# Kernel optimization log

Measured on AMD Instinct MI355X. Metric: run time of the kernel, lower is better.

## Reference

```python
import jax, jax.numpy as jnp
import numpy as np

N_NODES = 100000
BN_EPS = 1e-5


def _linear_params(key, fan_in, fan_out):
    k1, k2 = jax.random.split(key)
    lim = 1.0 / np.sqrt(fan_in)
    W = jax.random.uniform(k1, (fan_in, fan_out), jnp.float32, -lim, lim)
    b = jax.random.uniform(k2, (fan_out,), jnp.float32, -lim, lim)
    return W, b


def setup_inputs() -> dict:
    key = jax.random.key(0)
    ks = jax.random.split(key, 24)
    in_ch, hid, tdim, L = 17, 64, 32, 2
    E = 1600000
    inp = {}
    inp["x"] = jax.random.normal(ks[0], (N_NODES, in_ch), jnp.float32)
    inp["edge_index"] = jax.random.randint(ks[1], (2, E), 0, N_NODES, jnp.int64)
    inp["edge_dts"] = jax.random.uniform(ks[2], (E,), jnp.float32) * 100.0
    inp["batch_size"] = 10000
    # TimeEncode params (learned, TGAT init)
    inp["basis_freq"] = jnp.asarray(1.0 / 10 ** np.linspace(0, 9, tdim), jnp.float32)
    inp["phase"] = jnp.zeros((tdim,), jnp.float32)
    # TMP edge MLP: in = 2*in_ch + tdim
    mi = 2 * in_ch + tdim
    inp["tmp_W1"], inp["tmp_b1"] = _linear_params(ks[3], mi, mi // 2)
    inp["tmp_W2"], inp["tmp_b2"] = _linear_params(ks[4], mi // 2, in_ch)
    inp["proj_W"], inp["proj_b"] = _linear_params(ks[5], in_ch, hid)
    # SMP layers (stacked over L)
    si = 2 * hid
    W1s, b1s, W2s, b2s = [], [], [], []
    for l in range(L):
        W1, b1 = _linear_params(ks[6 + 2 * l], si, si // 2)
        W2, b2 = _linear_params(ks[7 + 2 * l], si // 2, hid)
        W1s.append(W1); b1s.append(b1); W2s.append(W2); b2s.append(b2)
    inp["smp_W1"] = jnp.stack(W1s); inp["smp_b1"] = jnp.stack(b1s)
    inp["smp_W2"] = jnp.stack(W2s); inp["smp_b2"] = jnp.stack(b2s)
    inp["bn_gamma"] = jnp.ones((L, hid), jnp.float32)
    inp["bn_beta"] = jnp.zeros((L, hid), jnp.float32)
    # classifier head
    inp["clf_W1"], inp["clf_b1"] = _linear_params(ks[12], hid, hid)
    inp["clf_g1"] = jnp.ones((hid,), jnp.float32); inp["clf_bb1"] = jnp.zeros((hid,), jnp.float32)
    inp["clf_W2"], inp["clf_b2"] = _linear_params(ks[13], hid, hid // 2)
    inp["clf_g2"] = jnp.ones((hid // 2,), jnp.float32); inp["clf_bb2"] = jnp.zeros((hid // 2,), jnp.float32)
    inp["clf_W3"], inp["clf_b3"] = _linear_params(ks[14], hid // 2, 1)
    return inp


def _segment_mean(vals, idx, n):
    s = jax.ops.segment_sum(vals, idx, num_segments=n)
    c = jax.ops.segment_sum(jnp.ones((idx.shape[0], 1), vals.dtype), idx, num_segments=n)
    return s / jnp.maximum(c, 1.0)


def _bn(x, g, b):
    m = x.mean(0)
    v = x.var(0)
    return (x - m) * jax.lax.rsqrt(v + BN_EPS) * g + b


def reference(x, edge_index, edge_dts, batch_size, basis_freq, phase,
              tmp_W1, tmp_b1, tmp_W2, tmp_b2, proj_W, proj_b,
              smp_W1, smp_b1, smp_W2, smp_b2, bn_gamma, bn_beta,
              clf_W1, clf_b1, clf_g1, clf_bb1,
              clf_W2, clf_b2, clf_g2, clf_bb2, clf_W3, clf_b3):
    src, dst = edge_index[0], edge_index[1]  # x_j = x[src], x_i = x[dst]
    n = x.shape[0]
    # TimeEncode: cos(t * freq + phase)  -> [E, time_dim]
    rel = jnp.cos(edge_dts[:, None] * basis_freq + phase)
    # --- TMP conv (applied once) ---
    x_i = x[dst]
    m_in = jnp.concatenate([x_i, x[src], rel], axis=-1)
    p = jnp.tanh(jax.nn.relu(m_in @ tmp_W1 + tmp_b1) @ tmp_W2 + tmp_b2)
    msg = (2.0 * p - 1.0) * x_i  # (p - q) * x_i with q = 1 - p
    h = x + _segment_mean(msg, dst, n)
    # --- project to hidden ---
    h = h @ proj_W + proj_b
    # --- L SMP layers with BatchNorm + ReLU (dropout = eval/identity) ---
    L = smp_W1.shape[0]
    for l in range(L):
        h_i = h[dst]
        m_in = jnp.concatenate([h_i, h[src]], axis=-1)
        p = jnp.tanh(jax.nn.relu(m_in @ smp_W1[l] + smp_b1[l]) @ smp_W2[l] + smp_b2[l])
        h = h + _segment_mean((2.0 * p - 1.0) * h_i, dst, n)
        h = jax.nn.relu(_bn(h, bn_gamma[l], bn_beta[l]))
    # --- classifier on seed nodes ---
    z = h[:batch_size]
    z = jax.nn.relu(_bn(z @ clf_W1 + clf_b1, clf_g1, clf_bb1))
    z = jax.nn.relu(_bn(z @ clf_W2 + clf_b2, clf_g2, clf_bb2))
    return z @ clf_W3 + clf_b3  # [batch_size, 1] logits
```

## Files before the change

kernel.cpp:

```cpp
#include <hip/hip_runtime.h>
#include <hip/hip_bf16.h>


typedef float  f32x4 __attribute__((ext_vector_type(4)));
typedef short  s16x8 __attribute__((ext_vector_type(8)));

__device__ __forceinline__ float tanh_factor(float u) {
  float e = __expf(2.0f * u);
  return fmaf(-4.0f, __builtin_amdgcn_rcpf(e + 1.0f), 1.0f);
}

__device__ __forceinline__ void atomic_add_f32(float* p, float v) {
  unsafeAtomicAdd(p, v);
}

__device__ __forceinline__ unsigned short f2bf(float f) {
  __hip_bfloat16 b = __float2bfloat16(f);
  return *(unsigned short*)&b;
}
__device__ __forceinline__ float bf2f(unsigned short u) {
  unsigned int v = ((unsigned int)u) << 16;
  return *(float*)&v;
}

__global__ __launch_bounds__(256) void k_hist(
    const int* __restrict__ ei, int* __restrict__ cntI, int E)
{
  int e = blockIdx.x * 256 + threadIdx.x;
  if (e < E) atomicAdd(&cntI[__builtin_nontemporal_load(ei + E + e)], 1);
}

__global__ __launch_bounds__(256) void k_scan_block(
    const int* __restrict__ cntI, int* __restrict__ cursor,
    int* __restrict__ bsum, int N)
{
  __shared__ int s[256];
  const int t = threadIdx.x;
  int i = blockIdx.x * 256 + t;
  int v = (i < N) ? cntI[i] : 0;
  s[t] = v;
  for (int off = 1; off < 256; off <<= 1) {
    __syncthreads();
    int x = (t >= off) ? s[t - off] : 0;
    __syncthreads();
    s[t] += x;
  }
  __syncthreads();
  if (i < N) cursor[i] = s[t] - v;
  if (t == 255) bsum[blockIdx.x] = s[255];
}

__global__ __launch_bounds__(512) void k_scan_bsum(int* __restrict__ bsum, int nb)
{
  __shared__ int s[512];
  const int t = threadIdx.x;
  int v = (t < nb) ? bsum[t] : 0;
  s[t] = v;
  for (int off = 1; off < 512; off <<= 1) {
    __syncthreads();
    int x = (t >= off) ? s[t - off] : 0;
    __syncthreads();
    s[t] += x;
  }
  __syncthreads();
  if (t < nb) bsum[t] = s[t] - v;
}

__global__ __launch_bounds__(256) void k_expand_add(
    int* __restrict__ cursor, const int* __restrict__ bsum,
    const int* __restrict__ cntI, int* __restrict__ dstS, int N)
{
  int n = blockIdx.x * 256 + threadIdx.x;
  if (n >= N) return;
  int cur = cursor[n] + bsum[blockIdx.x];
  cursor[n] = cur;
  int c = cntI[n];
  for (int i = 0; i < c; i++) dstS[cur + i] = n;
}

__global__ __launch_bounds__(256) void k_scatter_x(
    const int* __restrict__ ei, const float* __restrict__ dts,
    int* __restrict__ cursor, int2* __restrict__ srcdtS, int E, int N)
{
  const int g  = blockIdx.x & 7;
  const int bi = blockIdx.x >> 3;
  const int nb = gridDim.x >> 3;
  const int lo = (int)(((long long)N * g) >> 3);
  const int hi = (int)(((long long)N * (g + 1)) >> 3);
  for (int e = bi * 256 + threadIdx.x; e < E; e += nb * 256) {
    int d = __builtin_nontemporal_load(ei + E + e);
    if (d >= lo && d < hi) {
      int s = __builtin_nontemporal_load(ei + e);
      float dt = __builtin_nontemporal_load(dts + e);
      int pos = atomicAdd(&cursor[d], 1);
      srcdtS[pos] = make_int2(s, __float_as_int(dt));
    }
  }
}

__global__ __launch_bounds__(256) void prep_all(
    const float* __restrict__ x, const float* __restrict__ tW1,
    const float* __restrict__ tW2, const float* __restrict__ sW1,
    const float* __restrict__ sW2, const float* __restrict__ cW1,
    const float* __restrict__ cW2, unsigned short* __restrict__ xb,
    unsigned short* __restrict__ W1t1, unsigned short* __restrict__ W2t1,
    unsigned short* __restrict__ W1t, unsigned short* __restrict__ W2t,
    unsigned short* __restrict__ cW1t, unsigned short* __restrict__ cW2t, int N)
{
  int i = blockIdx.x * 256 + threadIdx.x;
  int totalX = N * 24;
  for (int idx = i; idx < totalX; idx += gridDim.x * 256) {
    int n = idx / 24, c = idx - n * 24;
    xb[idx] = (c < 17) ? f2bf(x[n * 17 + c]) : (unsigned short)0;
  }
  if (i < 48 * 96) {
    int n = i / 96, k = i - n * 96;
    int src = (k < 17) ? k : (k >= 24 && k < 41) ? (k - 24 + 17)
            : (k >= 48 && k < 80) ? (k - 48 + 34) : -1;
    W1t1[i] = (n < 33 && src >= 0) ? f2bf(tW1[src * 33 + n]) : (unsigned short)0;
  }
  if (i < 32 * 64) {
    int n = i / 64, k = i - n * 64;
    W2t1[i] = (n < 17 && k < 33) ? f2bf(tW2[k * 17 + n]) : (unsigned short)0;
  }
  if (i < 2 * 64 * 128) {
    int l = i >> 13; int r = i & 8191; int n = r >> 7; int k = r & 127;
    W1t[i] = f2bf(sW1[((size_t)l * 128 + k) * 64 + n]);
  }
  if (i < 2 * 64 * 64) {
    int l = i >> 12; int r = i & 4095; int n = r >> 6; int k = r & 63;
    W2t[i] = f2bf(sW2[((size_t)l * 64 + k) * 64 + n]);
  }
  if (i < 64 * 64) {
    int c = i >> 6, k = i & 63;
    cW1t[i] = f2bf(cW1[k * 64 + c]);
  }
  if (i < 32 * 64) {
    int c = i >> 6, k = i & 63;
    cW2t[i] = f2bf(cW2[k * 32 + c]);
  }
}

__global__ __launch_bounds__(256, 3) void phase1_edge_mfma(
    const unsigned short* __restrict__ xb, const int* __restrict__ dstS,
    const int2* __restrict__ srcdtS, const float* __restrict__ freq,
    const float* __restrict__ phs,
    const unsigned short* __restrict__ W1t1, const float* __restrict__ b1,
    const unsigned short* __restrict__ W2t1, const float* __restrict__ b2,
    float* __restrict__ accum, int E, int nwt)
{
  __shared__ unsigned short sA[64][104];
  __shared__ unsigned short sHid[64][72];
  __shared__ float sRed[64][20];
  __shared__ int   sDst[64];

  const int t = threadIdx.x;
  const int wv = t >> 6, lane = t & 63, l16 = lane & 15, quad = lane >> 4;
  const int r0 = wv * 16;
  const int e_loc = lane >> 2, q = lane & 3;
  const int rr = r0 + e_loc;

  s16x8 w1f[3][3], w2f[2][2];
  float bias1[3], bias2[2];
#pragma unroll
  for (int cb = 0; cb < 3; cb++) {
    int n = cb * 16 + l16;
#pragma unroll
    for (int kb = 0; kb < 3; kb++)
      w1f[cb][kb] = *(const s16x8*)&W1t1[n * 96 + kb * 32 + quad * 8];
    bias1[cb] = (n < 33) ? b1[n] : 0.0f;
  }
#pragma unroll
  for (int cb = 0; cb < 2; cb++) {
    int n = cb * 16 + l16;
#pragma unroll
    for (int kb = 0; kb < 2; kb++)
      w2f[cb][kb] = *(const s16x8*)&W2t1[n * 64 + kb * 32 + quad * 8];
    bias2[cb] = (n < 17) ? b2[n] : 0.0f;
  }

  float frq[8], phv[8];
#pragma unroll
  for (int j = 0; j < 8; j++) {
    frq[j] = freq[q * 8 + j];
    phv[j] = phs[q * 8 + j];
  }

  for (int i = lane; i < 16 * 28; i += 64) {
    int rrz = r0 + i / 28, c = i % 28;
    int col = (c < 6) ? 18 + c : (c < 12) ? 42 + (c - 6) : 80 + (c - 12);
    sA[rrz][col] = 0;
  }
  for (int i = lane; i < 256; i += 64)
    sHid[r0 + (i >> 4)][48 + (i & 15)] = 0;

  const int g8   = blockIdx.x & 7;
  const int tLo  = (int)(((long long)nwt * g8) >> 3);
  const int tHi  = (int)(((long long)nwt * (g8 + 1)) >> 3);
  const int wLoc = (blockIdx.x >> 3) * 4 + wv;
  const int nwLoc = (gridDim.x >> 3) * 4;

  int ndP = 0; uint4 xa0, xa1; unsigned int xa2 = 0; float dtP = 0.0f;
  auto issue = [&](int tt) {
    int er = (tt << 4) + e_loc; if (er >= E) er = E - 1;
    if (q < 2) {
      ndP = q ? srcdtS[er].x : dstS[er];
      const unsigned short* src = &xb[(size_t)ndP * 24];
      xa0 = *(const uint4*)&src[0];
      xa1 = *(const uint4*)&src[8];
      xa2 = *(const unsigned int*)&src[16];
    }
    dtP = __int_as_float(srcdtS[er].y);
  };
  {
    int t0 = tLo + wLoc; if (t0 >= nwt) t0 = nwt - 1;
    issue(t0);
  }

  for (int tile = tLo + wLoc; tile < tHi; tile += nwLoc) {
    const int eb = tile << 4;

    if (q < 2) {
      if (!q) sDst[rr] = ndP;
      const int base = q ? 24 : 0;
      *(uint4*)&sA[rr][base]     = xa0;
      *(uint4*)&sA[rr][base + 8] = xa1;
      *(unsigned int*)&sA[rr][base + 16] = xa2;
    }
    {
      unsigned short tmp[8] __attribute__((aligned(16)));
#pragma unroll
      for (int j = 0; j < 8; j++)
        tmp[j] = f2bf(__cosf(fmaf(dtP, frq[j], phv[j])));
      *(uint4*)&sA[rr][48 + q * 8] = *(const uint4*)&tmp[0];
    }

    { int nt = tile + nwLoc; issue(nt < tHi ? nt : tile); }

    f32x4 a1[3];
#pragma unroll
    for (int cb = 0; cb < 3; cb++)
      a1[cb] = (f32x4){bias1[cb], bias1[cb], bias1[cb], bias1[cb]};
#pragma unroll
    for (int kb = 0; kb < 3; kb++) {
      s16x8 aF = *(const s16x8*)&sA[r0 + l16][kb * 32 + quad * 8];
#pragma unroll
      for (int cb = 0; cb < 3; cb++)
        a1[cb] = __builtin_amdgcn_mfma_f32_16x16x32_bf16(aF, w1f[cb][kb], a1[cb], 0, 0, 0);
    }
#pragma unroll
    for (int cb = 0; cb < 3; cb++)
#pragma unroll
      for (int reg = 0; reg < 4; reg++)
        sHid[r0 + quad * 4 + reg][cb * 16 + l16] = f2bf(fmaxf(a1[cb][reg], 0.0f));

    f32x4 a2[2];
#pragma unroll
    for (int cb = 0; cb < 2; cb++)
      a2[cb] = (f32x4){bias2[cb], bias2[cb], bias2[cb], bias2[cb]};
#pragma unroll
    for (int kb = 0; kb < 2; kb++) {
      s16x8 aF = *(const s16x8*)&sHid[r0 + l16][kb * 32 + quad * 8];
#pragma unroll
      for (int cb = 0; cb < 2; cb++)
        a2[cb] = __builtin_amdgcn_mfma_f32_16x16x32_bf16(aF, w2f[cb][kb], a2[cb], 0, 0, 0);
    }

#pragma unroll
    for (int reg = 0; reg < 4; reg++) {
      int row = r0 + quad * 4 + reg;
      bool ok = (eb + quad * 4 + reg < E);
      sRed[row][l16] = ok ? tanh_factor(a2[0][reg]) : 0.0f;
      if (l16 == 0) sRed[row][16] = ok ? tanh_factor(a2[1][reg]) : 0.0f;
    }

    if (lane < 17) {
      int col = lane;
      float run = 0.0f;
      int cur = __builtin_amdgcn_readfirstlane(sDst[r0]);
#pragma unroll
      for (int k = 0; k < 16; k++) {
        int d = __builtin_amdgcn_readfirstlane(sDst[r0 + k]);
        float v = sRed[r0 + k][col];
        if (d != cur) {
          atomic_add_f32(&accum[(size_t)cur * 17 + col], run);
          run = 0.0f; cur = d;
        }
        run += v;
      }
      atomic_add_f32(&accum[(size_t)cur * 17 + col], run);
    }
  }
}

__global__ __launch_bounds__(256) void phase1_node(
    const float* __restrict__ x, const float* __restrict__ acc1,
    const int* __restrict__ cntI, const float* __restrict__ Wp,
    const float* __restrict__ bp, float* __restrict__ h,
    float* __restrict__ acc2, int N)
{
  __shared__ float s0[4][20];
  const int t = threadIdx.x;
  const int nb = blockIdx.x << 2;
  if (t < 68) {
    int nl = t / 17, c = t % 17;
    int n = nb + nl;
    float v = 0.0f;
    if (n < N) {
      float cnt = fmaxf((float)cntI[n], 1.0f);
      v = x[n * 17 + c] * (1.0f + acc1[n * 17 + c] / cnt);
    }
    s0[nl][c] = v;
  }
  __syncthreads();
  int nl = t >> 6, j = t & 63;
  int n = nb + nl;
  if (n < N) {
    float acc = bp[j];
#pragma unroll
    for (int c = 0; c < 17; c++) acc = fmaf(s0[nl][c], Wp[c * 64 + j], acc);
    h[n * 64 + j] = acc;
    acc2[n * 64 + j] = 0.0f;
  }
}

template <bool DO_BN>
__global__ void prep_P(
    float* __restrict__ h, const unsigned short* __restrict__ W1t,
    const float* __restrict__ b1,
    const float* __restrict__ bns, const float* __restrict__ bnq,
    const float* __restrict__ gam, const float* __restrict__ bet, float invR,
    unsigned short* __restrict__ P1, unsigned short* __restrict__ P2, int N)
{
  __shared__ unsigned short sH[64][72];
  __shared__ float sM[64], sS[64], sB[64];
  const int t = threadIdx.x;
  const int wv = t >> 6, lane = t & 63, l16 = lane & 15, quad = lane >> 4;
  const int nb = blockIdx.x << 6;

  if (DO_BN) {
    if (t < 64) {
      float m = bns[t] * invR;
      float var = bnq[t] * invR - m * m;
      sM[t] = m;
      sS[t] = gam[t] * rsqrtf(var + 1e-5f);
      sB[t] = bet[t];
    }
    __syncthreads();
  }

#pragma unroll
  for (int i = 0; i < 4; i++) {
    int g = t + i * 256;
    int r = g >> 4, c4 = (g & 15) << 2;
    int n0 = nb + r;
    bool valid = (n0 < N);
    int n = valid ? n0 : N - 1;
    float4 v = *(const float4*)&h[(size_t)n * 64 + c4];
    if (DO_BN) {
      v.x = fmaxf(fmaf(v.x - sM[c4 + 0], sS[c4 + 0], sB[c4 + 0]), 0.0f);
      v.y = fmaxf(fmaf(v.y - sM[c4 + 1], sS[c4 + 1], sB[c4 + 1]), 0.0f);
      v.z = fmaxf(fmaf(v.z - sM[c4 + 2], sS[c4 + 2], sB[c4 + 2]), 0.0f);
      v.w = fmaxf(fmaf(v.w - sM[c4 + 3], sS[c4 + 3], sB[c4 + 3]), 0.0f);
      if (valid) *(float4*)&h[(size_t)n0 * 64 + c4] = v;
    }
    ushort4 o = { f2bf(v.x), f2bf(v.y), f2bf(v.z), f2bf(v.w) };
    *(ushort4*)&sH[r][c4] = o;
  }
  __syncthreads();

  const int n = nb + wv * 16 + l16;
#pragma unroll
  for (int half = 0; half < 2; half++) {
    f32x4 acc[4];
#pragma unroll
    for (int cb = 0; cb < 4; cb++) {
      if (half == 0) {
        float4 bv = *(const float4*)&b1[cb * 16 + quad * 4];
        acc[cb] = (f32x4){bv.x, bv.y, bv.z, bv.w};
      } else {
        acc[cb] = (f32x4){0.0f, 0.0f, 0.0f, 0.0f};
      }
    }
#pragma unroll
    for (int kb = 0; kb < 2; kb++) {
      s16x8 bF = *(const s16x8*)&sH[wv * 16 + l16][kb * 32 + quad * 8];
#pragma unroll
      for (int cb = 0; cb < 4; cb++) {
        s16x8 aF = *(const s16x8*)&W1t[(cb * 16 + l16) * 128 + half * 64 + kb * 32 + quad * 8];
        acc[cb] = __builtin_amdgcn_mfma_f32_16x16x32_bf16(aF, bF, acc[cb], 0, 0, 0);
      }
    }
    if (n < N) {
      unsigned short* P = half ? P2 : P1;
#pragma unroll
      for (int cb = 0; cb < 4; cb++) {
        ushort4 o = { f2bf(acc[cb][0]), f2bf(acc[cb][1]),
                      f2bf(acc[cb][2]), f2bf(acc[cb][3]) };
        *(ushort4*)&P[(size_t)n * 64 + cb * 16 + quad * 4] = o;
      }
    }
  }
}

__global__ __launch_bounds__(256, 4) void phase2_edge(
    const unsigned short* __restrict__ P1, const unsigned short* __restrict__ P2,
    const int* __restrict__ dstS, const int2* __restrict__ srcdtS,
    const unsigned short* __restrict__ W2t, const float* __restrict__ b2,
    float* __restrict__ accum, int E, int nwt)
{
  __shared__ unsigned short sA[64][136];
  __shared__ int sDst[64];
  float* sRedF = (float*)&sA[0][0];

  const int t = threadIdx.x;
  const int wv = t >> 6, lane = t & 63, l16 = lane & 15, quad = lane >> 4;
  const int r0 = wv * 16;

  s16x8 w2f[4][2];
  f32x4 bias2v[4];
#pragma unroll
  for (int cb = 0; cb < 4; cb++) {
#pragma unroll
    for (int kb = 0; kb < 2; kb++)
      w2f[cb][kb] = *(const s16x8*)&W2t[(cb * 16 + l16) * 64 + kb * 32 + quad * 8];
    float4 bv = *(const float4*)&b2[cb * 16 + quad * 4];
    bias2v[cb] = (f32x4){bv.x, bv.y, bv.z, bv.w};
  }

  const int eRow = r0 + l16;

  const int e_loc = lane >> 2, q = lane & 3;
  const int rr = r0 + e_loc;
  const unsigned short* const Pb = (q < 2) ? P1 : P2;
  const int cb0 = q * 32;
  const size_t sub = (size_t)((q & 1) * 32);

  const int g8   = blockIdx.x & 7;
  const int tLo  = (int)(((long long)nwt * g8) >> 3);
  const int tHi  = (int)(((long long)nwt * (g8 + 1)) >> 3);
  const int wLoc = (blockIdx.x >> 3) * 4 + wv;
  const int nwLoc = (gridDim.x >> 3) * 4;

  int ndP = 0; uint4 pA, pB, pC, pD;
  auto issue = [&](int tt) {
    int er = (tt << 4) + e_loc; if (er >= E) er = E - 1;
    ndP = (q < 2) ? dstS[er] : srcdtS[er].x;
    const unsigned short* src = Pb + (size_t)ndP * 64 + sub;
    pA = *(const uint4*)&src[0];
    pB = *(const uint4*)&src[8];
    pC = *(const uint4*)&src[16];
    pD = *(const uint4*)&src[24];
  };
  {
    int t0 = tLo + wLoc; if (t0 >= nwt) t0 = nwt - 1;
    issue(t0);
  }

  for (int tile = tLo + wLoc; tile < tHi; tile += nwLoc) {
    const int eb = tile << 4;

    if (q == 0) sDst[rr] = ndP;
    *(uint4*)&sA[rr][cb0]      = pA;
    *(uint4*)&sA[rr][cb0 + 8]  = pB;
    *(uint4*)&sA[rr][cb0 + 16] = pC;
    *(uint4*)&sA[rr][cb0 + 24] = pD;

    { int nt = tile + nwLoc; issue(nt < tHi ? nt : tile); }

    s16x8 hidf[2];
#pragma unroll
    for (int kb = 0; kb < 2; kb++) {
      s16x8 x1 = *(const s16x8*)&sA[eRow][kb * 32 + quad * 8];
      s16x8 x2 = *(const s16x8*)&sA[eRow][64 + kb * 32 + quad * 8];
      s16x8 hf;
#pragma unroll
      for (int j = 0; j < 8; j++) {
        float a = bf2f((unsigned short)x1[j]);
        float b = bf2f((unsigned short)x2[j]);
        hf[j] = (short)f2bf(fmaxf(a + b, 0.0f));
      }
      hidf[kb] = hf;
    }

    f32x4 acc[4];
#pragma unroll
    for (int cb = 0; cb < 4; cb++) acc[cb] = bias2v[cb];
#pragma unroll
    for (int kb = 0; kb < 2; kb++)
#pragma unroll
      for (int cb = 0; cb < 4; cb++)
        acc[cb] = __builtin_amdgcn_mfma_f32_16x16x32_bf16(w2f[cb][kb], hidf[kb], acc[cb], 0, 0, 0);

    bool ok = (eb + l16 < E);
#pragma unroll
    for (int cb = 0; cb < 4; cb++) {
      f32x4 f;
#pragma unroll
      for (int reg = 0; reg < 4; reg++)
        f[reg] = ok ? tanh_factor(acc[cb][reg]) : 0.0f;
      *(f32x4*)&sRedF[eRow * 68 + cb * 16 + quad * 4] = f;
    }

    {
      float run = 0.0f;
      int cur = __builtin_amdgcn_readfirstlane(sDst[r0]);
#pragma unroll
      for (int k = 0; k < 16; k++) {
        int d = __builtin_amdgcn_readfirstlane(sDst[r0 + k]);
        float v = sRedF[(r0 + k) * 68 + lane];
        if (d != cur) {
          atomic_add_f32(&accum[(size_t)cur * 64 + lane], run);
          run = 0.0f; cur = d;
        }
        run += v;
      }
      atomic_add_f32(&accum[(size_t)cur * 64 + lane], run);
    }
  }
}

__global__ __launch_bounds__(256) void node_update_bn(
    float* __restrict__ h, float* __restrict__ accum,
    const int* __restrict__ cntI, float* __restrict__ bns,
    float* __restrict__ bnq, int N)
{
  const int t = threadIdx.x;
  float ls = 0.0f, lq = 0.0f;
  int total = N * 64;
  for (int idx = blockIdx.x * 256 + t; idx < total; idx += gridDim.x * 256) {
    int n = idx >> 6;
    float cnt = fmaxf((float)cntI[n], 1.0f);
    float v = h[idx] * (1.0f + accum[idx] / cnt);
    accum[idx] = 0.0f;
    h[idx] = v;
    ls += v; lq += v * v;
  }
  __shared__ float ss[256], sq[256];
  ss[t] = ls; sq[t] = lq;
  __syncthreads();
  if (t < 64) {
    float s = ss[t] + ss[t + 64] + ss[t + 128] + ss[t + 192];
    float q = sq[t] + sq[t + 64] + sq[t + 128] + sq[t + 192];
    atomic_add_f32(&bns[t], s);
    atomic_add_f32(&bnq[t], q);
  }
}

template <int NCB>
__global__ __launch_bounds__(256) void clf_mfma(
    const float* __restrict__ in, const unsigned short* __restrict__ Wt,
    const float* __restrict__ bias, float* __restrict__ z,
    float* __restrict__ bns, float* __restrict__ bnq,
    const float* __restrict__ ibns, const float* __restrict__ ibnq,
    const float* __restrict__ igam, const float* __restrict__ ibet,
    float iinvR, int rows)
{
  __shared__ unsigned short sIn[64][72];
  __shared__ float sM[64], sS[64], sB[64];
  const int t = threadIdx.x;
  const int wv = t >> 6, lane = t & 63, l16 = lane & 15, quad = lane >> 4;
  const int nb = blockIdx.x << 6;

  if (t < 64) {
    float m = ibns[t] * iinvR;
    float var = ibnq[t] * iinvR - m * m;
    sM[t] = m;
    sS[t] = igam[t] * rsqrtf(var + 1e-5f);
    sB[t] = ibet[t];
  }

  s16x8 wf[NCB][2];
  f32x4 bv[NCB];
#pragma unroll
  for (int cb = 0; cb < NCB; cb++) {
#pragma unroll
    for (int kb = 0; kb < 2; kb++)
      wf[cb][kb] = *(const s16x8*)&Wt[(cb * 16 + l16) * 64 + kb * 32 + quad * 8];
    float4 b4 = *(const float4*)&bias[cb * 16 + quad * 4];
    bv[cb] = (f32x4){b4.x, b4.y, b4.z, b4.w};
  }
  __syncthreads();

#pragma unroll
  for (int i = 0; i < 4; i++) {
    int g = t + i * 256;
    int r = g >> 4, c4 = (g & 15) << 2;
    int n = nb + r; if (n >= rows) n = rows - 1;
    float4 v = *(const float4*)&in[(size_t)n * 64 + c4];
    v.x = fmaxf(fmaf(v.x - sM[c4 + 0], sS[c4 + 0], sB[c4 + 0]), 0.0f);
    v.y = fmaxf(fmaf(v.y - sM[c4 + 1], sS[c4 + 1], sB[c4 + 1]), 0.0f);
    v.z = fmaxf(fmaf(v.z - sM[c4 + 2], sS[c4 + 2], sB[c4 + 2]), 0.0f);
    v.w = fmaxf(fmaf(v.w - sM[c4 + 3], sS[c4 + 3], sB[c4 + 3]), 0.0f);
    ushort4 o = { f2bf(v.x), f2bf(v.y), f2bf(v.z), f2bf(v.w) };
    *(ushort4*)&sIn[r][c4] = o;
  }
  __syncthreads();

  const int n = nb + wv * 16 + l16;
  const bool ok = (n < rows);
  f32x4 acc[NCB];
#pragma unroll
  for (int cb = 0; cb < NCB; cb++) acc[cb] = bv[cb];
#pragma unroll
  for (int kb = 0; kb < 2; kb++) {
    s16x8 bF = *(const s16x8*)&sIn[wv * 16 + l16][kb * 32 + quad * 8];
#pragma unroll
    for (int cb = 0; cb < NCB; cb++)
      acc[cb] = __builtin_amdgcn_mfma_f32_16x16x32_bf16(wf[cb][kb], bF, acc[cb], 0, 0, 0);
  }

#pragma unroll
  for (int cb = 0; cb < NCB; cb++) {
    if (ok)
      *(float4*)&z[(size_t)n * (NCB * 16) + cb * 16 + quad * 4] =
          make_float4(acc[cb][0], acc[cb][1], acc[cb][2], acc[cb][3]);
    f32x4 s, q;
#pragma unroll
    for (int reg = 0; reg < 4; reg++) {
      float v = ok ? acc[cb][reg] : 0.0f;
      s[reg] = v; q[reg] = v * v;
    }
#pragma unroll
    for (int m = 1; m < 16; m <<= 1) {
#pragma unroll
      for (int reg = 0; reg < 4; reg++) {
        s[reg] += __shfl_xor(s[reg], m);
        q[reg] += __shfl_xor(q[reg], m);
      }
    }
    if (l16 == 0) {
#pragma unroll
      for (int reg = 0; reg < 4; reg++) {
        int col = cb * 16 + quad * 4 + reg;
        atomic_add_f32(&bns[col], s[reg]);
        atomic_add_f32(&bnq[col], q[reg]);
      }
    }
  }
}

__global__ __launch_bounds__(256) void clf_final(
    const float* __restrict__ z2, const float* __restrict__ W3,
    const float* __restrict__ b3,
    const float* __restrict__ ibns, const float* __restrict__ ibnq,
    const float* __restrict__ igam, const float* __restrict__ ibet,
    float iinvR, float* __restrict__ out, int rows)
{
  __shared__ float sM[32], sS[32], sB[32];
  const int t = threadIdx.x;
  if (t < 32) {
    float m = ibns[t] * iinvR;
    float var = ibnq[t] * iinvR - m * m;
    sM[t] = m;
    sS[t] = igam[t] * rsqrtf(var + 1e-5f);
    sB[t] = ibet[t];
  }
  __syncthreads();
  int n = blockIdx.x * 256 + t;
  if (n >= rows) return;
  float acc = b3[0];
#pragma unroll
  for (int k = 0; k < 32; k++) {
    float v = fmaxf(fmaf(z2[n * 32 + k] - sM[k], sS[k], sB[k]), 0.0f);
    acc = fmaf(v, W3[k], acc);
  }
  out[n] = acc;
}

extern "C" void kernel_launch(void* const* d_in, const int* in_sizes, int n_in,
                              void* d_out, int out_size, void* d_ws, size_t ws_size,
                              hipStream_t stream)
{
  const float* x    = (const float*)d_in[0];
  const int*   ei   = (const int*)  d_in[1];
  const float* dts  = (const float*)d_in[2];
  const float* freq = (const float*)d_in[4];
  const float* phs  = (const float*)d_in[5];
  const float* tW1  = (const float*)d_in[6];
  const float* tb1  = (const float*)d_in[7];
  const float* tW2  = (const float*)d_in[8];
  const float* tb2  = (const float*)d_in[9];
  const float* pW   = (const float*)d_in[10];
  const float* pb   = (const float*)d_in[11];
  const float* sW1  = (const float*)d_in[12];
  const float* sb1  = (const float*)d_in[13];
  const float* sW2  = (const float*)d_in[14];
  const float* sb2  = (const float*)d_in[15];
  const float* bng  = (const float*)d_in[16];
  const float* bnb  = (const float*)d_in[17];
  const float* cW1  = (const float*)d_in[18];
  const float* cb1  = (const float*)d_in[19];
  const float* cg1  = (const float*)d_in[20];
  const float* cbb1 = (const float*)d_in[21];
  const float* cW2  = (const float*)d_in[22];
  const float* cb2  = (const float*)d_in[23];
  const float* cg2  = (const float*)d_in[24];
  const float* cbb2 = (const float*)d_in[25];
  const float* cW3  = (const float*)d_in[26];
  const float* cb3  = (const float*)d_in[27];
  float* out = (float*)d_out;

  const int N = in_sizes[0] / 17;
  const int E = in_sizes[1] / 2;
  const int B = out_size;

  char* base = (char*)d_ws;
  size_t off = 0;
  float* h    = (float*)(base + off); off += (size_t)N * 64 * 4;
  float* acc2 = (float*)(base + off); off += (size_t)N * 64 * 4;
  char*  uni  = base + off;           off += (size_t)N * 64 * 4;
  float* bnsAll = (float*)(base + off); off += 8 * 64 * 4;
  unsigned short* W1t = (unsigned short*)(base + off); off += 2 * 64 * 128 * 2;
  unsigned short* W2t = (unsigned short*)(base + off); off += 2 * 64 * 64 * 2;
  unsigned short* cW1t = (unsigned short*)(base + off); off += 64 * 64 * 2;
  unsigned short* cW2t = (unsigned short*)(base + off); off += 32 * 64 * 2;
  int* cntI   = (int*)(base + off); off += (size_t)N * 4;
  int* cursor = (int*)(base + off); off += (size_t)N * 4;
  int* bsum   = (int*)(base + off); off += 512 * 4;
  int* dstS   = (int*)(base + off); off += (size_t)E * 4;
  off = (off + 15) & ~(size_t)15;
  int2* srcdtS = (int2*)(base + off); off += (size_t)E * 8;
  size_t needed = off;
  if (ws_size < needed) return;

  float* acc1 = (float*)uni;
  unsigned short* xb   = (unsigned short*)(uni + (size_t)N * 17 * 4);
  unsigned short* W1t1 = xb + (size_t)N * 24;
  unsigned short* W2t1 = W1t1 + 48 * 96;
  unsigned short* P1 = (unsigned short*)uni;
  unsigned short* P2 = P1 + (size_t)N * 64;
  float* z1 = (float*)uni;
  float* z2 = z1 + (size_t)B * 64;

  const int nwt = (E + 15) / 16;
  const int NB = (N + 255) / 256;
  if (NB > 512) return;

  hipMemsetAsync(cntI, 0, (size_t)N * 4, stream);
  hipMemsetAsync(acc1, 0, (size_t)N * 17 * 4, stream);
  hipMemsetAsync(bnsAll, 0, 8 * 64 * 4, stream);

  k_hist<<<(E + 255) / 256, 256, 0, stream>>>(ei, cntI, E);
  k_scan_block<<<NB, 256, 0, stream>>>(cntI, cursor, bsum, N);
  k_scan_bsum<<<1, 512, 0, stream>>>(bsum, NB);
  k_expand_add<<<NB, 256, 0, stream>>>(cursor, bsum, cntI, dstS, N);
  k_scatter_x<<<1024, 256, 0, stream>>>(ei, dts, cursor, srcdtS, E, N);
  prep_all<<<(N * 24 + 255) / 256, 256, 0, stream>>>(
      x, tW1, tW2, sW1, sW2, cW1, cW2, xb, W1t1, W2t1, W1t, W2t, cW1t, cW2t, N);

  phase1_edge_mfma<<<768, 256, 0, stream>>>(
      xb, dstS, srcdtS, freq, phs, W1t1, tb1, W2t1, tb2, acc1, E, nwt);
  phase1_node<<<(N + 3) / 4, 256, 0, stream>>>(x, acc1, cntI, pW, pb, h, acc2, N);

  const int PB = (N + 63) / 64;
  prep_P<false><<<PB, 256, 0, stream>>>(
      h, W1t, sb1, nullptr, nullptr, nullptr, nullptr, 0.0f, P1, P2, N);
  phase2_edge<<<1024, 256, 0, stream>>>(
      P1, P2, dstS, srcdtS, W2t, sb2, acc2, E, nwt);
  node_update_bn<<<1024, 256, 0, stream>>>(h, acc2, cntI,
                                           bnsAll + 0, bnsAll + 64, N);
  prep_P<true><<<PB, 256, 0, stream>>>(
      h, W1t + (size_t)64 * 128, sb1 + 64, bnsAll + 0, bnsAll + 64,
      bng, bnb, 1.0f / (float)N, P1, P2, N);
  phase2_edge<<<1024, 256, 0, stream>>>(
      P1, P2, dstS, srcdtS, W2t + (size_t)64 * 64, sb2 + 64, acc2, E, nwt);
  node_update_bn<<<1024, 256, 0, stream>>>(h, acc2, cntI,
                                           bnsAll + 128, bnsAll + 192, N);

  const int CB = (B + 63) / 64;
  clf_mfma<4><<<CB, 256, 0, stream>>>(
      h, cW1t, cb1, z1, bnsAll + 256, bnsAll + 320,
      bnsAll + 128, bnsAll + 192, bng + 64, bnb + 64, 1.0f / (float)N, B);
  clf_mfma<2><<<CB, 256, 0, stream>>>(
      z1, cW2t, cb2, z2, bnsAll + 384, bnsAll + 448,
      bnsAll + 256, bnsAll + 320, cg1, cbb1, 1.0f / (float)B, B);
  clf_final<<<(B + 255) / 256, 256, 0, stream>>>(
      z2, cW3, cb3, bnsAll + 384, bnsAll + 448, cg2, cbb2,
      1.0f / (float)B, out, B);
}
```

Baseline: 814.1 us.

## Deepen edge-kernel prefetch to two stages and raise occupancy and grid size

Both edge kernels now fetch indices two tiles ahead and the gathered node payload one tile ahead. The index load is no longer serialized with the dependent gather in the same prefetch step. Launch bounds go up (phase1 3→4, phase2 4→5 blocks per CU), and the grids grow to match. This is meant to hide the latency of the dependent index→gather chain. The extra live registers under a tighter register cap could cause spills.

Result: no change. 800.1 us (-1.7%).

```diff
diff --git a/kernel.cpp b/kernel.cpp
--- a/kernel.cpp
+++ b/kernel.cpp
@@ -141,7 +141,7 @@
   }
 }
 
-__global__ __launch_bounds__(256, 3) void phase1_edge_mfma(
+__global__ __launch_bounds__(256, 4) void phase1_edge_mfma(
     const unsigned short* __restrict__ xb, const int* __restrict__ dstS,
     const int2* __restrict__ srcdtS, const float* __restrict__ freq,
     const float* __restrict__ phs,
@@ -200,21 +200,29 @@
   const int wLoc = (blockIdx.x >> 3) * 4 + wv;
   const int nwLoc = (gridDim.x >> 3) * 4;
 
+  int idxN = 0; float dtN = 0.0f;
   int ndP = 0; uint4 xa0, xa1; unsigned int xa2 = 0; float dtP = 0.0f;
-  auto issue = [&](int tt) {
+  auto issue_idx = [&](int tt) {
     int er = (tt << 4) + e_loc; if (er >= E) er = E - 1;
+    int2 sd = srcdtS[er];
+    idxN = q ? sd.x : dstS[er];
+    dtN  = __int_as_float(sd.y);
+  };
+  auto issue_payload = [&]() {
+    ndP = idxN; dtP = dtN;
     if (q < 2) {
-      ndP = q ? srcdtS[er].x : dstS[er];
       const unsigned short* src = &xb[(size_t)ndP * 24];
       xa0 = *(const uint4*)&src[0];
       xa1 = *(const uint4*)&src[8];
       xa2 = *(const unsigned int*)&src[16];
     }
-    dtP = __int_as_float(srcdtS[er].y);
   };
   {
     int t0 = tLo + wLoc; if (t0 >= nwt) t0 = nwt - 1;
-    issue(t0);
+    issue_idx(t0);
+    issue_payload();
+    int t1 = t0 + nwLoc; if (t1 >= tHi) t1 = t0;
+    issue_idx(t1);
   }
 
   for (int tile = tLo + wLoc; tile < tHi; tile += nwLoc) {
@@ -235,7 +243,8 @@
       *(uint4*)&sA[rr][48 + q * 8] = *(const uint4*)&tmp[0];
     }
 
-    { int nt = tile + nwLoc; issue(nt < tHi ? nt : tile); }
+    issue_payload();
+    { int nt = tile + 2 * nwLoc; issue_idx(nt < tHi ? nt : tile); }
 
     f32x4 a1[3];
 #pragma unroll
@@ -403,7 +412,7 @@
   }
 }
 
-__global__ __launch_bounds__(256, 4) void phase2_edge(
+__global__ __launch_bounds__(256, 5) void phase2_edge(
     const unsigned short* __restrict__ P1, const unsigned short* __restrict__ P2,
     const int* __restrict__ dstS, const int2* __restrict__ srcdtS,
     const unsigned short* __restrict__ W2t, const float* __restrict__ b2,
@@ -442,10 +451,14 @@
   const int wLoc = (blockIdx.x >> 3) * 4 + wv;
   const int nwLoc = (gridDim.x >> 3) * 4;
 
+  int idxN = 0;
   int ndP = 0; uint4 pA, pB, pC, pD;
-  auto issue = [&](int tt) {
+  auto issue_idx = [&](int tt) {
     int er = (tt << 4) + e_loc; if (er >= E) er = E - 1;
-    ndP = (q < 2) ? dstS[er] : srcdtS[er].x;
+    idxN = (q < 2) ? dstS[er] : srcdtS[er].x;
+  };
+  auto issue_payload = [&]() {
+    ndP = idxN;
     const unsigned short* src = Pb + (size_t)ndP * 64 + sub;
     pA = *(const uint4*)&src[0];
     pB = *(const uint4*)&src[8];
@@ -454,7 +467,10 @@
   };
   {
     int t0 = tLo + wLoc; if (t0 >= nwt) t0 = nwt - 1;
-    issue(t0);
+    issue_idx(t0);
+    issue_payload();
+    int t1 = t0 + nwLoc; if (t1 >= tHi) t1 = t0;
+    issue_idx(t1);
   }
 
   for (int tile = tLo + wLoc; tile < tHi; tile += nwLoc) {
@@ -466,7 +482,8 @@
     *(uint4*)&sA[rr][cb0 + 16] = pC;
     *(uint4*)&sA[rr][cb0 + 24] = pD;
 
-    { int nt = tile + nwLoc; issue(nt < tHi ? nt : tile); }
+    issue_payload();
+    { int nt = tile + 2 * nwLoc; issue_idx(nt < tHi ? nt : tile); }
 
     s16x8 hidf[2];
 #pragma unroll
@@ -749,21 +766,21 @@
   prep_all<<<(N * 24 + 255) / 256, 256, 0, stream>>>(
       x, tW1, tW2, sW1, sW2, cW1, cW2, xb, W1t1, W2t1, W1t, W2t, cW1t, cW2t, N);
 
-  phase1_edge_mfma<<<768, 256, 0, stream>>>(
+  phase1_edge_mfma<<<1024, 256, 0, stream>>>(
       xb, dstS, srcdtS, freq, phs, W1t1, tb1, W2t1, tb2, acc1, E, nwt);
   phase1_node<<<(N + 3) / 4, 256, 0, stream>>>(x, acc1, cntI, pW, pb, h, acc2, N);
 
   const int PB = (N + 63) / 64;
   prep_P<false><<<PB, 256, 0, stream>>>(
       h, W1t, sb1, nullptr, nullptr, nullptr, nullptr, 0.0f, P1, P2, N);
-  phase2_edge<<<1024, 256, 0, stream>>>(
+  phase2_edge<<<1280, 256, 0, stream>>>(
       P1, P2, dstS, srcdtS, W2t, sb2, acc2, E, nwt);
   node_update_bn<<<1024, 256, 0, stream>>>(h, acc2, cntI,
                                            bnsAll + 0, bnsAll + 64, N);
   prep_P<true><<<PB, 256, 0, stream>>>(
       h, W1t + (size_t)64 * 128, sb1 + 64, bnsAll + 0, bnsAll + 64,
       bng, bnb, 1.0f / (float)N, P1, P2, N);
-  phase2_edge<<<1024, 256, 0, stream>>>(
+  phase2_edge<<<1280, 256, 0, stream>>>(
       P1, P2, dstS, srcdtS, W2t + (size_t)64 * 64, sb2 + 64, acc2, E, nwt);
   node_update_bn<<<1024, 256, 0, stream>>>(h, acc2, cntI,
                                            bnsAll + 128, bnsAll + 192, N);
```

## Deepen gather prefetch pipeline in edge kernels with two tiles in flight

Applied to the files above, without the earlier changes.

Both edge kernels now process tile pairs per iteration. They keep two payload gathers in flight and prefetch the index loads two steps ahead, so the dependent index-then-payload gather latency is hidden better. phase2_edge also raises its occupancy hint to 5 blocks per SM and launches 1280 blocks instead of 1024. The deeper pipeline costs more registers, and that could hurt occupancy or cause spills. The work split changes too, with each wave starting at tLo+2*wLoc and striding by 2*S.

Result: slower. 982.1 us (+20.6%).

```diff
diff --git a/kernel.cpp b/kernel.cpp
--- a/kernel.cpp
+++ b/kernel.cpp
@@ -198,97 +198,184 @@
   const int tLo  = (int)(((long long)nwt * g8) >> 3);
   const int tHi  = (int)(((long long)nwt * (g8 + 1)) >> 3);
   const int wLoc = (blockIdx.x >> 3) * 4 + wv;
-  const int nwLoc = (gridDim.x >> 3) * 4;
-
-  int ndP = 0; uint4 xa0, xa1; unsigned int xa2 = 0; float dtP = 0.0f;
-  auto issue = [&](int tt) {
+  const int S    = (gridDim.x >> 3) * 4;
+  const int tp0  = tLo + 2 * wLoc;
+
+  int iA = 0, iB = 0, jA = 0, jB = 0;
+  float dA = 0.0f, dB = 0.0f, eA = 0.0f, eB = 0.0f;
+  uint4 a0 = {0,0,0,0}, a1 = {0,0,0,0}, b0 = {0,0,0,0}, b1v = {0,0,0,0};
+  unsigned int a2v = 0, b2v = 0;
+
+  auto clampT = [&](int tt) { return tt < tHi ? tt : tHi - 1; };
+  auto ld_idx = [&](int tt, int& ix, float& dt) {
     int er = (tt << 4) + e_loc; if (er >= E) er = E - 1;
+    int2 sd = srcdtS[er];
+    ix = q ? sd.x : dstS[er];
+    dt = __int_as_float(sd.y);
+  };
+  auto ld_pay = [&](int ix, uint4& x0, uint4& x1, unsigned int& x2) {
     if (q < 2) {
-      ndP = q ? srcdtS[er].x : dstS[er];
-      const unsigned short* src = &xb[(size_t)ndP * 24];
-      xa0 = *(const uint4*)&src[0];
-      xa1 = *(const uint4*)&src[8];
-      xa2 = *(const unsigned int*)&src[16];
-    }
-    dtP = __int_as_float(srcdtS[er].y);
+      const unsigned short* src = &xb[(size_t)ix * 24];
+      x0 = *(const uint4*)&src[0];
+      x1 = *(const uint4*)&src[8];
+      x2 = *(const unsigned int*)&src[16];
+    }
   };
-  {
-    int t0 = tLo + wLoc; if (t0 >= nwt) t0 = nwt - 1;
-    issue(t0);
-  }
-
-  for (int tile = tLo + wLoc; tile < tHi; tile += nwLoc) {
-    const int eb = tile << 4;
-
-    if (q < 2) {
-      if (!q) sDst[rr] = ndP;
-      const int base = q ? 24 : 0;
-      *(uint4*)&sA[rr][base]     = xa0;
-      *(uint4*)&sA[rr][base + 8] = xa1;
-      *(unsigned int*)&sA[rr][base + 16] = xa2;
-    }
+
+  if (tp0 < tHi) {
+    ld_idx(tp0, iA, dA);
+    ld_idx(clampT(tp0 + 1), iB, dB);
+    ld_pay(iA, a0, a1, a2v);
+    ld_pay(iB, b0, b1v, b2v);
+    ld_idx(clampT(tp0 + 2 * S), jA, eA);
+    ld_idx(clampT(tp0 + 2 * S + 1), jB, eB);
+  }
+
+  for (int tp = tp0; tp < tHi; tp += 2 * S) {
     {
+      if (q < 2) {
+        if (!q) sDst[rr] = iA;
+        const int base = q ? 24 : 0;
+        *(uint4*)&sA[rr][base]     = a0;
+        *(uint4*)&sA[rr][base + 8] = a1;
+        *(unsigned int*)&sA[rr][base + 16] = a2v;
+      }
       unsigned short tmp[8] __attribute__((aligned(16)));
 #pragma unroll
       for (int j = 0; j < 8; j++)
-        tmp[j] = f2bf(__cosf(fmaf(dtP, frq[j], phv[j])));
+        tmp[j] = f2bf(__cosf(fmaf(dA, frq[j], phv[j])));
       *(uint4*)&sA[rr][48 + q * 8] = *(const uint4*)&tmp[0];
     }
-
-    { int nt = tile + nwLoc; issue(nt < tHi ? nt : tile); }
-
-    f32x4 a1[3];
-#pragma unroll
-    for (int cb = 0; cb < 3; cb++)
-      a1[cb] = (f32x4){bias1[cb], bias1[cb], bias1[cb], bias1[cb]};
-#pragma unroll
-    for (int kb = 0; kb < 3; kb++) {
-      s16x8 aF = *(const s16x8*)&sA[r0 + l16][kb * 32 + quad * 8];
+    ld_pay(jA, a0, a1, a2v); iA = jA; dA = eA;
+    ld_idx(clampT(tp + 4 * S), jA, eA);
+
+    {
+      const int eb = tp << 4;
+      f32x4 p1[3];
 #pragma unroll
       for (int cb = 0; cb < 3; cb++)
-        a1[cb] = __builtin_amdgcn_mfma_f32_16x16x32_bf16(aF, w1f[cb][kb], a1[cb], 0, 0, 0);
-    }
-#pragma unroll
-    for (int cb = 0; cb < 3; cb++)
-#pragma unroll
-      for (int reg = 0; reg < 4; reg++)
-        sHid[r0 + quad * 4 + reg][cb * 16 + l16] = f2bf(fmaxf(a1[cb][reg], 0.0f));
-
-    f32x4 a2[2];
-#pragma unroll
-    for (int cb = 0; cb < 2; cb++)
-      a2[cb] = (f32x4){bias2[cb], bias2[cb], bias2[cb], bias2[cb]};
-#pragma unroll
-    for (int kb = 0; kb < 2; kb++) {
-      s16x8 aF = *(const s16x8*)&sHid[r0 + l16][kb * 32 + quad * 8];
+        p1[cb] = (f32x4){bias1[cb], bias1[cb], bias1[cb], bias1[cb]};
+#pragma unroll
+      for (int kb = 0; kb < 3; kb++) {
+        s16x8 aF = *(const s16x8*)&sA[r0 + l16][kb * 32 + quad * 8];
+#pragma unroll
+        for (int cb = 0; cb < 3; cb++)
+          p1[cb] = __builtin_amdgcn_mfma_f32_16x16x32_bf16(aF, w1f[cb][kb], p1[cb], 0, 0, 0);
+      }
+#pragma unroll
+      for (int cb = 0; cb < 3; cb++)
+#pragma unroll
+        for (int reg = 0; reg < 4; reg++)
+          sHid[r0 + quad * 4 + reg][cb * 16 + l16] = f2bf(fmaxf(p1[cb][reg], 0.0f));
+
+      f32x4 p2[2];
 #pragma unroll
       for (int cb = 0; cb < 2; cb++)
-        a2[cb] = __builtin_amdgcn_mfma_f32_16x16x32_bf16(aF, w2f[cb][kb], a2[cb], 0, 0, 0);
-    }
-
-#pragma unroll
-    for (int reg = 0; reg < 4; reg++) {
-      int row = r0 + quad * 4 + reg;
-      bool ok = (eb + quad * 4 + reg < E);
-      sRed[row][l16] = ok ? tanh_factor(a2[0][reg]) : 0.0f;
-      if (l16 == 0) sRed[row][16] = ok ? tanh_factor(a2[1][reg]) : 0.0f;
-    }
-
-    if (lane < 17) {
-      int col = lane;
-      float run = 0.0f;
-      int cur = __builtin_amdgcn_readfirstlane(sDst[r0]);
-#pragma unroll
-      for (int k = 0; k < 16; k++) {
-        int d = __builtin_amdgcn_readfirstlane(sDst[r0 + k]);
-        float v = sRed[r0 + k][col];
-        if (d != cur) {
+        p2[cb] = (f32x4){bias2[cb], bias2[cb], bias2[cb], bias2[cb]};
+#pragma unroll
+      for (int kb = 0; kb < 2; kb++) {
+        s16x8 aF = *(const s16x8*)&sHid[r0 + l16][kb * 32 + quad * 8];
+#pragma unroll
+        for (int cb = 0; cb < 2; cb++)
+          p2[cb] = __builtin_amdgcn_mfma_f32_16x16x32_bf16(aF, w2f[cb][kb], p2[cb], 0, 0, 0);
+      }
+#pragma unroll
+      for (int reg = 0; reg < 4; reg++) {
+        int row = r0 + quad * 4 + reg;
+        bool ok = (eb + quad * 4 + reg < E);
+        sRed[row][l16] = ok ? tanh_factor(p2[0][reg]) : 0.0f;
+        if (l16 == 0) sRed[row][16] = ok ? tanh_factor(p2[1][reg]) : 0.0f;
+      }
+      if (lane < 17) {
+        int col = lane;
+        float run = 0.0f;
+        int cur = __builtin_amdgcn_readfirstlane(sDst[r0]);
+#pragma unroll
+        for (int k = 0; k < 16; k++) {
+          int d = __builtin_amdgcn_readfirstlane(sDst[r0 + k]);
+          float v = sRed[r0 + k][col];
+          if (d != cur) {
+            atomic_add_f32(&accum[(size_t)cur * 17 + col], run);
+            run = 0.0f; cur = d;
+          }
+          run += v;
+        }
+        atomic_add_f32(&accum[(size_t)cur * 17 + col], run);
+      }
+    }
+
+    if (tp + 1 < tHi) {
+      {
+        if (q < 2) {
+          if (!q) sDst[rr] = iB;
+          const int base = q ? 24 : 0;
+          *(uint4*)&sA[rr][base]     = b0;
+          *(uint4*)&sA[rr][base + 8] = b1v;
+          *(unsigned int*)&sA[rr][base + 16] = b2v;
+        }
+        unsigned short tmp[8] __attribute__((aligned(16)));
+#pragma unroll
+        for (int j = 0; j < 8; j++)
+          tmp[j] = f2bf(__cosf(fmaf(dB, frq[j], phv[j])));
+        *(uint4*)&sA[rr][48 + q * 8] = *(const uint4*)&tmp[0];
+      }
+      ld_pay(jB, b0, b1v, b2v); iB = jB; dB = eB;
+      ld_idx(clampT(tp + 4 * S + 1), jB, eB);
+
+      {
+        const int eb = (tp + 1) << 4;
+        f32x4 p1[3];
+#pragma unroll
+        for (int cb = 0; cb < 3; cb++)
+          p1[cb] = (f32x4){bias1[cb], bias1[cb], bias1[cb], bias1[cb]};
+#pragma unroll
+        for (int kb = 0; kb < 3; kb++) {
+          s16x8 aF = *(const s16x8*)&sA[r0 + l16][kb * 32 + quad * 8];
+#pragma unroll
+          for (int cb = 0; cb < 3; cb++)
+            p1[cb] = __builtin_amdgcn_mfma_f32_16x16x32_bf16(aF, w1f[cb][kb], p1[cb], 0, 0, 0);
+        }
+#pragma unroll
+        for (int cb = 0; cb < 3; cb++)
+#pragma unroll
+          for (int reg = 0; reg < 4; reg++)
+            sHid[r0 + quad * 4 + reg][cb * 16 + l16] = f2bf(fmaxf(p1[cb][reg], 0.0f));
+
+        f32x4 p2[2];
+#pragma unroll
+        for (int cb = 0; cb < 2; cb++)
+          p2[cb] = (f32x4){bias2[cb], bias2[cb], bias2[cb], bias2[cb]};
+#pragma unroll
+        for (int kb = 0; kb < 2; kb++) {
+          s16x8 aF = *(const s16x8*)&sHid[r0 + l16][kb * 32 + quad * 8];
+#pragma unroll
+          for (int cb = 0; cb < 2; cb++)
+            p2[cb] = __builtin_amdgcn_mfma_f32_16x16x32_bf16(aF, w2f[cb][kb], p2[cb], 0, 0, 0);
+        }
+#pragma unroll
+        for (int reg = 0; reg < 4; reg++) {
+          int row = r0 + quad * 4 + reg;
+          bool ok = (eb + quad * 4 + reg < E);
+          sRed[row][l16] = ok ? tanh_factor(p2[0][reg]) : 0.0f;
+          if (l16 == 0) sRed[row][16] = ok ? tanh_factor(p2[1][reg]) : 0.0f;
+        }
+        if (lane < 17) {
+          int col = lane;
+          float run = 0.0f;
+          int cur = __builtin_amdgcn_readfirstlane(sDst[r0]);
+#pragma unroll
+          for (int k = 0; k < 16; k++) {
+            int d = __builtin_amdgcn_readfirstlane(sDst[r0 + k]);
+            float v = sRed[r0 + k][col];
+            if (d != cur) {
+              atomic_add_f32(&accum[(size_t)cur * 17 + col], run);
+              run = 0.0f; cur = d;
+            }
+            run += v;
+          }
           atomic_add_f32(&accum[(size_t)cur * 17 + col], run);
-          run = 0.0f; cur = d;
-        }
-        run += v;
-      }
-      atomic_add_f32(&accum[(size_t)cur * 17 + col], run);
+        }
+      }
     }
   }
 }
@@ -403,7 +490,7 @@
   }
 }
 
-__global__ __launch_bounds__(256, 4) void phase2_edge(
+__global__ __launch_bounds__(256, 5) void phase2_edge(
     const unsigned short* __restrict__ P1, const unsigned short* __restrict__ P2,
     const int* __restrict__ dstS, const int2* __restrict__ srcdtS,
     const unsigned short* __restrict__ W2t, const float* __restrict__ b2,
@@ -429,7 +516,6 @@
   }
 
   const int eRow = r0 + l16;
-
   const int e_loc = lane >> 2, q = lane & 3;
   const int rr = r0 + e_loc;
   const unsigned short* const Pb = (q < 2) ? P1 : P2;
@@ -440,82 +526,155 @@
   const int tLo  = (int)(((long long)nwt * g8) >> 3);
   const int tHi  = (int)(((long long)nwt * (g8 + 1)) >> 3);
   const int wLoc = (blockIdx.x >> 3) * 4 + wv;
-  const int nwLoc = (gridDim.x >> 3) * 4;
-
-  int ndP = 0; uint4 pA, pB, pC, pD;
-  auto issue = [&](int tt) {
+  const int S    = (gridDim.x >> 3) * 4;
+  const int tp0  = tLo + 2 * wLoc;
+
+  int iA = 0, iB = 0, jA = 0, jB = 0;
+  uint4 pa0, pa1, pa2, pa3, pb0, pb1, pb2, pb3;
+
+  auto clampT = [&](int tt) { return tt < tHi ? tt : tHi - 1; };
+  auto ld_idx = [&](int tt, int& ix) {
     int er = (tt << 4) + e_loc; if (er >= E) er = E - 1;
-    ndP = (q < 2) ? dstS[er] : srcdtS[er].x;
-    const unsigned short* src = Pb + (size_t)ndP * 64 + sub;
-    pA = *(const uint4*)&src[0];
-    pB = *(const uint4*)&src[8];
-    pC = *(const uint4*)&src[16];
-    pD = *(const uint4*)&src[24];
+    ix = (q < 2) ? dstS[er] : srcdtS[er].x;
   };
-  {
-    int t0 = tLo + wLoc; if (t0 >= nwt) t0 = nwt - 1;
-    issue(t0);
-  }
-
-  for (int tile = tLo + wLoc; tile < tHi; tile += nwLoc) {
-    const int eb = tile << 4;
-
-    if (q == 0) sDst[rr] = ndP;
-    *(uint4*)&sA[rr][cb0]      = pA;
-    *(uint4*)&sA[rr][cb0 + 8]  = pB;
-    *(uint4*)&sA[rr][cb0 + 16] = pC;
-    *(uint4*)&sA[rr][cb0 + 24] = pD;
-
-    { int nt = tile + nwLoc; issue(nt < tHi ? nt : tile); }
-
-    s16x8 hidf[2];
-#pragma unroll
-    for (int kb = 0; kb < 2; kb++) {
-      s16x8 x1 = *(const s16x8*)&sA[eRow][kb * 32 + quad * 8];
-      s16x8 x2 = *(const s16x8*)&sA[eRow][64 + kb * 32 + quad * 8];
-      s16x8 hf;
-#pragma unroll
-      for (int j = 0; j < 8; j++) {
-        float a = bf2f((unsigned short)x1[j]);
-        float b = bf2f((unsigned short)x2[j]);
-        hf[j] = (short)f2bf(fmaxf(a + b, 0.0f));
-      }
-      hidf[kb] = hf;
-    }
-
-    f32x4 acc[4];
-#pragma unroll
-    for (int cb = 0; cb < 4; cb++) acc[cb] = bias2v[cb];
-#pragma unroll
-    for (int kb = 0; kb < 2; kb++)
-#pragma unroll
-      for (int cb = 0; cb < 4; cb++)
-        acc[cb] = __builtin_amdgcn_mfma_f32_16x16x32_bf16(w2f[cb][kb], hidf[kb], acc[cb], 0, 0, 0);
-
-    bool ok = (eb + l16 < E);
-#pragma unroll
-    for (int cb = 0; cb < 4; cb++) {
-      f32x4 f;
-#pragma unroll
-      for (int reg = 0; reg < 4; reg++)
-        f[reg] = ok ? tanh_factor(acc[cb][reg]) : 0.0f;
-      *(f32x4*)&sRedF[eRow * 68 + cb * 16 + quad * 4] = f;
-    }
+  auto ld_pay = [&](int ix, uint4& x0, uint4& x1, uint4& x2, uint4& x3) {
+    const unsigned short* src = Pb + (size_t)ix * 64 + sub;
+    x0 = *(const uint4*)&src[0];
+    x1 = *(const uint4*)&src[8];
+    x2 = *(const uint4*)&src[16];
+    x3 = *(const uint4*)&src[24];
+  };
+
+  if (tp0 < tHi) {
+    ld_idx(tp0, iA);
+    ld_idx(clampT(tp0 + 1), iB);
+    ld_pay(iA, pa0, pa1, pa2, pa3);
+    ld_pay(iB, pb0, pb1, pb2, pb3);
+    ld_idx(clampT(tp0 + 2 * S), jA);
+    ld_idx(clampT(tp0 + 2 * S + 1), jB);
+  }
+
+  for (int tp = tp0; tp < tHi; tp += 2 * S) {
+    if (q == 0) sDst[rr] = iA;
+    *(uint4*)&sA[rr][cb0]      = pa0;
+    *(uint4*)&sA[rr][cb0 + 8]  = pa1;
+    *(uint4*)&sA[rr][cb0 + 16] = pa2;
+    *(uint4*)&sA[rr][cb0 + 24] = pa3;
+
+    ld_pay(jA, pa0, pa1, pa2, pa3); iA = jA;
+    ld_idx(clampT(tp + 4 * S), jA);
 
     {
-      float run = 0.0f;
-      int cur = __builtin_amdgcn_readfirstlane(sDst[r0]);
-#pragma unroll
-      for (int k = 0; k < 16; k++) {
-        int d = __builtin_amdgcn_readfirstlane(sDst[r0 + k]);
-        float v = sRedF[(r0 + k) * 68 + lane];
-        if (d != cur) {
+      const int eb = tp << 4;
+      s16x8 hidf[2];
+#pragma unroll
+      for (int kb = 0; kb < 2; kb++) {
+        s16x8 x1 = *(const s16x8*)&sA[eRow][kb * 32 + quad * 8];
+        s16x8 x2 = *(const s16x8*)&sA[eRow][64 + kb * 32 + quad * 8];
+        s16x8 hf;
+#pragma unroll
+        for (int j = 0; j < 8; j++) {
+          float a = bf2f((unsigned short)x1[j]);
+          float b = bf2f((unsigned short)x2[j]);
+          hf[j] = (short)f2bf(fmaxf(a + b, 0.0f));
+        }
+        hidf[kb] = hf;
+      }
+      f32x4 acc[4];
+#pragma unroll
+      for (int cb = 0; cb < 4; cb++) acc[cb] = bias2v[cb];
+#pragma unroll
+      for (int kb = 0; kb < 2; kb++)
+#pragma unroll
+        for (int cb = 0; cb < 4; cb++)
+          acc[cb] = __builtin_amdgcn_mfma_f32_16x16x32_bf16(w2f[cb][kb], hidf[kb], acc[cb], 0, 0, 0);
+
+      bool ok = (eb + l16 < E);
+#pragma unroll
+      for (int cb = 0; cb < 4; cb++) {
+        f32x4 f;
+#pragma unroll
+        for (int reg = 0; reg < 4; reg++)
+          f[reg] = ok ? tanh_factor(acc[cb][reg]) : 0.0f;
+        *(f32x4*)&sRedF[eRow * 68 + cb * 16 + quad * 4] = f;
+      }
+      {
+        float run = 0.0f;
+        int cur = __builtin_amdgcn_readfirstlane(sDst[r0]);
+#pragma unroll
+        for (int k = 0; k < 16; k++) {
+          int d = __builtin_amdgcn_readfirstlane(sDst[r0 + k]);
+          float v = sRedF[(r0 + k) * 68 + lane];
+          if (d != cur) {
+            atomic_add_f32(&accum[(size_t)cur * 64 + lane], run);
+            run = 0.0f; cur = d;
+          }
+          run += v;
+        }
+        atomic_add_f32(&accum[(size_t)cur * 64 + lane], run);
+      }
+    }
+
+    if (tp + 1 < tHi) {
+      if (q == 0) sDst[rr] = iB;
+      *(uint4*)&sA[rr][cb0]      = pb0;
+      *(uint4*)&sA[rr][cb0 + 8]  = pb1;
+      *(uint4*)&sA[rr][cb0 + 16] = pb2;
+      *(uint4*)&sA[rr][cb0 + 24] = pb3;
+
+      ld_pay(jB, pb0, pb1, pb2, pb3); iB = jB;
+      ld_idx(clampT(tp + 4 * S + 1), jB);
+
+      {
+        const int eb = (tp + 1) << 4;
+        s16x8 hidf[2];
+#pragma unroll
+        for (int kb = 0; kb < 2; kb++) {
+          s16x8 x1 = *(const s16x8*)&sA[eRow][kb * 32 + quad * 8];
+          s16x8 x2 = *(const s16x8*)&sA[eRow][64 + kb * 32 + quad * 8];
+          s16x8 hf;
+#pragma unroll
+          for (int j = 0; j < 8; j++) {
+            float a = bf2f((unsigned short)x1[j]);
+            float b = bf2f((unsigned short)x2[j]);
+            hf[j] = (short)f2bf(fmaxf(a + b, 0.0f));
+          }
+          hidf[kb] = hf;
+        }
+        f32x4 acc[4];
+#pragma unroll
+        for (int cb = 0; cb < 4; cb++) acc[cb] = bias2v[cb];
+#pragma unroll
+        for (int kb = 0; kb < 2; kb++)
+#pragma unroll
+          for (int cb = 0; cb < 4; cb++)
+            acc[cb] = __builtin_amdgcn_mfma_f32_16x16x32_bf16(w2f[cb][kb], hidf[kb], acc[cb], 0, 0, 0);
+
+        bool ok = (eb + l16 < E);
+#pragma unroll
+        for (int cb = 0; cb < 4; cb++) {
+          f32x4 f;
+#pragma unroll
+          for (int reg = 0; reg < 4; reg++)
+            f[reg] = ok ? tanh_factor(acc[cb][reg]) : 0.0f;
+          *(f32x4*)&sRedF[eRow * 68 + cb * 16 + quad * 4] = f;
+        }
+        {
+          float run = 0.0f;
+          int cur = __builtin_amdgcn_readfirstlane(sDst[r0]);
+#pragma unroll
+          for (int k = 0; k < 16; k++) {
+            int d = __builtin_amdgcn_readfirstlane(sDst[r0 + k]);
+            float v = sRedF[(r0 + k) * 68 + lane];
+            if (d != cur) {
+              atomic_add_f32(&accum[(size_t)cur * 64 + lane], run);
+              run = 0.0f; cur = d;
+            }
+            run += v;
+          }
           atomic_add_f32(&accum[(size_t)cur * 64 + lane], run);
-          run = 0.0f; cur = d;
-        }
-        run += v;
-      }
-      atomic_add_f32(&accum[(size_t)cur * 64 + lane], run);
+        }
+      }
     }
   }
 }
@@ -756,14 +915,14 @@
   const int PB = (N + 63) / 64;
   prep_P<false><<<PB, 256, 0, stream>>>(
       h, W1t, sb1, nullptr, nullptr, nullptr, nullptr, 0.0f, P1, P2, N);
-  phase2_edge<<<1024, 256, 0, stream>>>(
+  phase2_edge<<<1280, 256, 0, stream>>>(
       P1, P2, dstS, srcdtS, W2t, sb2, acc2, E, nwt);
   node_update_bn<<<1024, 256, 0, stream>>>(h, acc2, cntI,
                                            bnsAll + 0, bnsAll + 64, N);
   prep_P<true><<<PB, 256, 0, stream>>>(
       h, W1t + (size_t)64 * 128, sb1 + 64, bnsAll + 0, bnsAll + 64,
       bng, bnb, 1.0f / (float)N, P1, P2, N);
-  phase2_edge<<<1024, 256, 0, stream>>>(
+  phase2_edge<<<1280, 256, 0, stream>>>(
       P1, P2, dstS, srcdtS, W2t + (size_t)64 * 64, sb2 + 64, acc2, E, nwt);
   node_update_bn<<<1024, 256, 0, stream>>>(h, acc2, cntI,
                                            bnsAll + 128, bnsAll + 192, N);
```
